# Performance work log

Hardware: AMD Instinct MI355X
Metric: run time of the kernel (lower is better)

## Reference

```python
import jax, jax.numpy as jnp
import numpy as np

B, L, E, D = 4, 4096, 768, 64

def setup_inputs() -> dict:
    key = jax.random.key(0)
    ks = jax.random.split(key, 7)
    x = jax.random.normal(ks[0], (B, L, E), dtype=jnp.float32)
    # True = masked (strict upper triangle), as in masked_fill semantics
    causal_mask = jnp.triu(jnp.ones((L, L), dtype=bool), k=1)
    # True = valid token (inverted with ~ inside forward); all valid to avoid NaN rows
    pad_mask = jnp.ones((B, L), dtype=bool)
    s = 1.0 / np.sqrt(E)
    Wk = jax.random.uniform(ks[1], (E, D), jnp.float32, -s, s)
    bk = jax.random.uniform(ks[2], (D,), jnp.float32, -s, s)
    Wq = jax.random.uniform(ks[3], (E, D), jnp.float32, -s, s)
    bq = jax.random.uniform(ks[4], (D,), jnp.float32, -s, s)
    Wv = jax.random.uniform(ks[5], (E, D), jnp.float32, -s, s)
    bv = jax.random.uniform(ks[6], (D,), jnp.float32, -s, s)
    return {"x": x, "causal_mask": causal_mask, "pad_mask": pad_mask,
            "Wk": Wk, "bk": bk, "Wq": Wq, "bq": bq, "Wv": Wv, "bv": bv}

def reference(x, causal_mask, pad_mask, Wk, bk, Wq, bq, Wv, bv):
    # Linear projections: [B,L,E] @ [E,D] + [D]
    K = jnp.einsum('ble,ed->bld', x, Wk) + bk
    Q = jnp.einsum('ble,ed->bld', x, Wq) + bq
    V = jnp.einsum('ble,ed->bld', x, Wv) + bv
    d = Q.shape[-1]
    scores = jnp.einsum('bqd,bkd->bqk', Q, K) / jnp.sqrt(jnp.asarray(d, Q.dtype))
    # full_mask: causal (True=masked) OR key-position padding (~pad_mask, broadcast over query dim)
    full_mask = causal_mask[None, :, :] | (~pad_mask)[:, None, :]
    scores = jnp.where(full_mask, -jnp.inf, scores)
    attn = jax.nn.softmax(scores, axis=-1)
    out = jnp.einsum('bqk,bkd->bqd', attn, V)
    return out
```

## Files before the change

### kernel.cpp

```cpp
#include <hip/hip_runtime.h>

#define L_SEQ 4096
#define BATCH 4
#define EDIM 768

typedef __attribute__((ext_vector_type(8))) short bf16x8;
typedef __attribute__((ext_vector_type(4))) float f32x4;
typedef __attribute__((ext_vector_type(16))) float f32x16;
typedef __attribute__((ext_vector_type(4))) unsigned short u16x4;
typedef __attribute__((ext_vector_type(8))) unsigned short u16x8;
typedef __attribute__((ext_vector_type(2))) _Float16 f16x2;
typedef __attribute__((ext_vector_type(4))) _Float16 f16x4;

#define QSCALE (0.125f * 1.4426950408889634f)

__device__ __forceinline__ unsigned short f2bf(float f) {
  unsigned u = __builtin_bit_cast(unsigned, f);
  u += 0x7FFFu + ((u >> 16) & 1u);
  return (unsigned short)(u >> 16);
}

__device__ __forceinline__ f16x4 half_of(u16x8 v, int h) {
  u16x4 t = h ? (u16x4){v[4], v[5], v[6], v[7]} : (u16x4){v[0], v[1], v[2], v[3]};
  return __builtin_bit_cast(f16x4, t);
}

__device__ __forceinline__ f16x2 pkrtz(float a, float b) {
  return __builtin_bit_cast(f16x2, __builtin_amdgcn_cvt_pkrtz(a, b));
}

__global__ __launch_bounds__(256) void prep_kernel(
    const float* __restrict__ Wq, const float* __restrict__ Wk,
    const float* __restrict__ Wv, unsigned short* __restrict__ WT) {
  int g = blockIdx.x * 256 + threadIdx.x;
  if (g >= 192 * EDIM) return;
  int row = g / EDIM, k = g - row * EDIM;
  int z = row >> 6, n = row & 63;
  const float* W = (z == 0) ? Wq : (z == 1) ? Wk : Wv;
  WT[g] = f2bf(W[k * 64 + n]);
}

__global__ __launch_bounds__(512) void proj_kernel(
    const float* __restrict__ x, const unsigned short* __restrict__ WT,
    const float* __restrict__ bq, const float* __restrict__ bk, const float* __restrict__ bv,
    unsigned short* __restrict__ Qf, unsigned short* __restrict__ Kf,
    unsigned short* __restrict__ Vf) {
  __shared__ unsigned short SH[2 * 13824];
  int tid = threadIdx.x;
  int w = tid >> 6, lane = tid & 63, l15 = lane & 15, g4 = lane >> 4;
  int rq = w & 3, ch = w >> 2;
  int m0 = blockIdx.x * 64;
  int brow = tid >> 3, bsg = tid & 7;

  f32x4 acc[6];
#pragma unroll
  for (int cf = 0; cf < 6; cf++) acc[cf] = (f32x4){0.f, 0.f, 0.f, 0.f};

  f32x4 arA[4], arB[4];
  u16x8 brA[3], brB[3];

  auto loadA = [&](f32x4 (&ar)[4], int k0) {
    const float* xp = x + (size_t)(m0 + 16 * rq + l15) * EDIM + k0 + g4 * 8;
    ar[0] = *(const f32x4*)xp;
    ar[1] = *(const f32x4*)(xp + 4);
    ar[2] = *(const f32x4*)(xp + 32);
    ar[3] = *(const f32x4*)(xp + 36);
  };
  auto loadB = [&](u16x8 (&br)[3], int k0) {
#pragma unroll
    for (int pp = 0; pp < 3; pp++)
      br[pp] = *(const u16x8*)(WT + (size_t)(brow + pp * 64) * EDIM + k0 + bsg * 8);
  };
  auto writeB = [&](int cur, u16x8 (&br)[3]) {
#pragma unroll
    for (int pp = 0; pp < 3; pp++)
      *(u16x8*)&SH[cur * 13824 + (brow + pp * 64) * 72 + bsg * 8] = br[pp];
  };
  auto mkfrag = [&](f32x4 lo, f32x4 hi) {
    union { u16x8 u; bf16x8 b; } r;
    r.u[0] = f2bf(lo[0]); r.u[1] = f2bf(lo[1]); r.u[2] = f2bf(lo[2]); r.u[3] = f2bf(lo[3]);
    r.u[4] = f2bf(hi[0]); r.u[5] = f2bf(hi[1]); r.u[6] = f2bf(hi[2]); r.u[7] = f2bf(hi[3]);
    return r.b;
  };
  auto compute = [&](int cur, f32x4 (&ar)[4]) {
#pragma unroll
    for (int ks = 0; ks < 2; ks++) {
      bf16x8 a = mkfrag(ar[ks * 2], ar[ks * 2 + 1]);
#pragma unroll
      for (int cf = 0; cf < 6; cf++) {
        bf16x8 bb = *(const bf16x8*)&SH[cur * 13824 + (ch * 96 + cf * 16 + l15) * 72 +
                                        ks * 32 + g4 * 8];
        acc[cf] = __builtin_amdgcn_mfma_f32_16x16x32_bf16(a, bb, acc[cf], 0, 0, 0);
      }
    }
  };

  loadA(arA, 0);
  loadB(brA, 0);
  for (int ss = 0; ss < 6; ss++) {
    int k1 = (2 * ss + 1) * 64;
    loadA(arB, k1);
    loadB(brB, k1);
    writeB(0, brA);
    __syncthreads();
    compute(0, arA);
    if (ss < 5) {
      int k2 = (2 * ss + 2) * 64;
      loadA(arA, k2);
      loadB(brA, k2);
    }
    writeB(1, brB);
    __syncthreads();
    compute(1, arB);
  }

  __syncthreads();
  unsigned short* LQ = SH;
  unsigned short* LK = SH + 4096;
  unsigned short* LV = SH + 8192;
#pragma unroll
  for (int cf = 0; cf < 6; cf++) {
    int c = ch * 96 + cf * 16 + l15;
    int z = c >> 6, d = c & 63;
    float bb_ = (z == 0) ? bq[d] : (z == 1) ? bk[d] : bv[d];
#pragma unroll
    for (int r = 0; r < 4; r++) {
      int t = 16 * rq + g4 * 4 + r;
      int sl = t >> 5, tl = t & 31;
      float v = acc[cf][r] + bb_;
      if (z == 2) {
        int fv = sl * 2048 + (d >> 5) * 1024 + ((tl >> 4) & 1) * 512 +
                 ((d & 31) + ((tl >> 2) & 1) * 32) * 8 + ((tl >> 3) & 1) * 4 + (tl & 3);
        _Float16 hv = (_Float16)v;
        LV[fv] = __builtin_bit_cast(unsigned short, hv);
      } else {
        int fqk = sl * 2048 + (d >> 4) * 512 + (tl + ((d >> 3) & 1) * 32) * 8 + (d & 7);
        if (z == 0) LQ[fqk] = f2bf(v * QSCALE);
        else        LK[fqk] = f2bf(v);
      }
    }
  }
  __syncthreads();
  {
    int b_ = m0 >> 12;
    int S0 = (m0 >> 5) & 127;
    size_t base = ((size_t)(b_ * 128 + S0)) * 2048;
    ((u16x8*)(Qf + base))[tid] = ((const u16x8*)LQ)[tid];
    ((u16x8*)(Kf + base))[tid] = ((const u16x8*)LK)[tid];
    ((u16x8*)(Vf + base))[tid] = ((const u16x8*)LV)[tid];
  }
}

__global__ __launch_bounds__(512, 2) void attn_kernel(
    const unsigned short* __restrict__ Qf, const unsigned short* __restrict__ Kf,
    const unsigned short* __restrict__ Vf, float* __restrict__ out) {
  __shared__ float OB[8][32][68];
  __shared__ float ML[8][2][32];
  int tid = threadIdx.x;
  int w = tid >> 6, lane = tid & 63;
  int ql = lane & 31, hi = lane >> 5;
  int blk = blockIdx.x;
  int xcd = blk & 7;
  int b = xcd >> 1;
  int pid = ((xcd & 1) << 5) | (blk >> 3);
  int sA = pid, sB = 127 - pid;
  size_t bL = (size_t)b * L_SEQ;
  const unsigned short* Qb = Qf + (size_t)b * 128 * 2048;
  const unsigned short* Kb = Kf + (size_t)b * 128 * 2048;
  const unsigned short* Vb = Vf + (size_t)b * 128 * 2048;

  bf16x8 qA[4], qB[4];
#pragma unroll
  for (int kh = 0; kh < 4; kh++) {
    qA[kh] = *(const bf16x8*)(Qb + ((size_t)sA * 4 + kh) * 512 + lane * 8);
    qB[kh] = *(const bf16x8*)(Qb + ((size_t)sB * 4 + kh) * 512 + lane * 8);
  }
  f32x16 oA0, oA1, oB0, oB1;
#pragma unroll
  for (int i = 0; i < 16; i++) { oA0[i] = 0.f; oA1[i] = 0.f; oB0[i] = 0.f; oB1[i] = 0.f; }
  float mA = -1e38f, lA = 0.f, mB = -1e38f, lB = 0.f;

  auto loadK = [&](bf16x8 (&kf)[4], int j) {
    const unsigned short* kp = Kb + (size_t)j * 2048 + lane * 8;
#pragma unroll
    for (int q = 0; q < 4; q++) kf[q] = *(const bf16x8*)(kp + q * 512);
  };
  auto loadV = [&](u16x8 (&vf)[4], int j) {
    const unsigned short* vp = Vb + (size_t)j * 2048 + lane * 8;
#pragma unroll
    for (int q = 0; q < 4; q++) vf[q] = *(const u16x8*)(vp + q * 512);
  };

  auto strip = [&](bf16x8 (&kf)[4], u16x8 (&vf)[4], int j, int s, bf16x8 (&qf)[4],
                   f32x16& o0, f32x16& o1, float& m, float& l) {
    f32x16 st;
#pragma unroll
    for (int i = 0; i < 16; i++) st[i] = 0.f;
    __builtin_amdgcn_s_setprio(1);
#pragma unroll
    for (int kh = 0; kh < 4; kh++)
      st = __builtin_amdgcn_mfma_f32_32x32x16_bf16(kf[kh], qf[kh], st, 0, 0, 0);
    __builtin_amdgcn_s_setprio(0);

    if (j == s) {
#pragma unroll
      for (int r = 0; r < 16; r++) {
        int tl = (r & 3) + 8 * (r >> 2) + 4 * hi;
        if (tl > ql) st[r] = -1e30f;
      }
    }

    float mx = st[0];
#pragma unroll
    for (int r = 1; r < 16; r++) mx = fmaxf(mx, st[r]);
    mx = fmaxf(mx, __shfl_xor(mx, 32));
    if (!__all(mx <= m + 11.0f)) {
      float mn = fmaxf(m, mx);
      float sc = exp2f(m - mn);
      m = mn; l *= sc;
#pragma unroll
      for (int i = 0; i < 16; i++) { o0[i] *= sc; o1[i] *= sc; }
    }
    float rs = 0.f;
#pragma unroll
    for (int r = 0; r < 16; r++) { st[r] = exp2f(st[r] - m); rs += st[r]; }
    rs += __shfl_xor(rs, 32);
    l += rs;

    f16x4 pb[4];
#pragma unroll
    for (int oc = 0; oc < 4; oc++) {
      f16x2 a = pkrtz(st[4 * oc], st[4 * oc + 1]);
      f16x2 c = pkrtz(st[4 * oc + 2], st[4 * oc + 3]);
      pb[oc] = (f16x4){a[0], a[1], c[0], c[1]};
    }
    __builtin_amdgcn_s_setprio(1);
#pragma unroll
    for (int oc = 0; oc < 4; oc++)
      o0 = __builtin_amdgcn_mfma_f32_32x32x8f16(half_of(vf[oc >> 1], oc & 1), pb[oc], o0, 0, 0, 0);
#pragma unroll
    for (int oc = 0; oc < 4; oc++)
      o1 = __builtin_amdgcn_mfma_f32_32x32x8f16(half_of(vf[2 + (oc >> 1)], oc & 1), pb[oc], o1, 0, 0, 0);
    __builtin_amdgcn_s_setprio(0);
  };

  bf16x8 kfA[4], kfB[4];
  u16x8 vfA[4], vfB[4];
  {
    int j = w;
    loadK(kfA, j);
    loadV(vfA, j);
    while (true) {
      int jn = j + 8;
      bool hasB = (jn <= sB);
      if (hasB) loadK(kfB, jn);
      if (j <= sA) strip(kfA, vfA, j, sA, qA, oA0, oA1, mA, lA);
      if (hasB) loadV(vfB, jn);
      strip(kfA, vfA, j, sB, qB, oB0, oB1, mB, lB);
      if (!hasB) break;
      j = jn;
      jn = j + 8;
      bool hasA = (jn <= sB);
      if (hasA) loadK(kfA, jn);
      if (j <= sA) strip(kfB, vfB, j, sA, qA, oA0, oA1, mA, lA);
      if (hasA) loadV(vfA, jn);
      strip(kfB, vfB, j, sB, qB, oB0, oB1, mB, lB);
      if (!hasA) break;
      j = jn;
    }
  }

  auto stash_reduce = [&](int s, f32x16& o0, f32x16& o1, float m, float l) {
    __syncthreads();
#pragma unroll
    for (int g = 0; g < 4; g++) {
      *(f32x4*)&OB[w][ql][8 * g + 4 * hi] =
          (f32x4){o0[4 * g], o0[4 * g + 1], o0[4 * g + 2], o0[4 * g + 3]};
      *(f32x4*)&OB[w][ql][32 + 8 * g + 4 * hi] =
          (f32x4){o1[4 * g], o1[4 * g + 1], o1[4 * g + 2], o1[4 * g + 3]};
    }
    if (hi == 0) { ML[w][0][ql] = m; ML[w][1][ql] = l; }
    __syncthreads();
    int q = tid >> 4, dg = tid & 15;
    float mw[8], lw[8];
    float ms = -1e38f;
#pragma unroll
    for (int ww = 0; ww < 8; ww++) {
      mw[ww] = ML[ww][0][q]; lw[ww] = ML[ww][1][q];
      ms = fmaxf(ms, mw[ww]);
    }
    float denom = 0.f, ew[8];
#pragma unroll
    for (int ww = 0; ww < 8; ww++) { ew[ww] = exp2f(mw[ww] - ms); denom += lw[ww] * ew[ww]; }
    float inv = 1.0f / denom;
    f32x4 acc = (f32x4){0.f, 0.f, 0.f, 0.f};
#pragma unroll
    for (int ww = 0; ww < 8; ww++) {
      f32x4 v = *(const f32x4*)&OB[ww][q][dg * 4];
      acc += v * ew[ww];
    }
    acc *= inv;
    *(f32x4*)(out + (bL + (size_t)s * 32 + q) * 64 + dg * 4) = acc;
  };
  stash_reduce(sA, oA0, oA1, mA, lA);
  stash_reduce(sB, oB0, oB1, mB, lB);
}

extern "C" void kernel_launch(void* const* d_in, const int* in_sizes, int n_in,
                              void* d_out, int out_size, void* d_ws, size_t ws_size,
                              hipStream_t stream) {
  const float* x  = (const float*)d_in[0];
  const float* Wk = (const float*)d_in[3];
  const float* bk = (const float*)d_in[4];
  const float* Wq = (const float*)d_in[5];
  const float* bq = (const float*)d_in[6];
  const float* Wv = (const float*)d_in[7];
  const float* bv = (const float*)d_in[8];
  float* out = (float*)d_out;

  char* ws = (char*)d_ws;
  unsigned short* WT = (unsigned short*)ws;
  unsigned short* Qf = (unsigned short*)(ws + 294912);
  unsigned short* Kf = (unsigned short*)(ws + 294912 + 2097152);
  unsigned short* Vf = (unsigned short*)(ws + 294912 + 2 * 2097152);

  prep_kernel<<<576, 256, 0, stream>>>(Wq, Wk, Wv, WT);
  proj_kernel<<<256, 512, 0, stream>>>(x, WT, bq, bk, bv, Qf, Kf, Vf);
  attn_kernel<<<256, 512, 0, stream>>>(Qf, Kf, Vf, out);
}
```

Measured before the change: 53.89 us.

## Load projection weights directly from global and switch softmax to natural exp

The projection kernel drops the LDS staging of bf16 weights and the per-stage barriers, reading B fragments straight from global/L2, and triple-buffers the x loads across a fully unrolled K loop. The Q scale no longer folds in log2(e); softmax uses __expf in place of exp2f and the rescale threshold drops from 11 to 8. The attention loop issues the K and V loads together rather than splitting them around the strips. This removes the LDS writes and syncs in the projection, but adds redundant global weight reads per wave and extra multiplies inside __expf, which lowers to exp2 of a scaled input.

```diff
diff --git a/kernel.cpp b/kernel.cpp
--- a/kernel.cpp
+++ b/kernel.cpp
@@ -11,8 +11,6 @@
 typedef __attribute__((ext_vector_type(8))) unsigned short u16x8;
 typedef __attribute__((ext_vector_type(2))) _Float16 f16x2;
 typedef __attribute__((ext_vector_type(4))) _Float16 f16x4;
-
-#define QSCALE (0.125f * 1.4426950408889634f)
 
 __device__ __forceinline__ unsigned short f2bf(float f) {
   unsigned u = __builtin_bit_cast(unsigned, f);
@@ -45,36 +43,26 @@
     const float* __restrict__ bq, const float* __restrict__ bk, const float* __restrict__ bv,
     unsigned short* __restrict__ Qf, unsigned short* __restrict__ Kf,
     unsigned short* __restrict__ Vf) {
-  __shared__ unsigned short SH[2 * 13824];
+  __shared__ unsigned short SH[12288];
   int tid = threadIdx.x;
   int w = tid >> 6, lane = tid & 63, l15 = lane & 15, g4 = lane >> 4;
   int rq = w & 3, ch = w >> 2;
   int m0 = blockIdx.x * 64;
-  int brow = tid >> 3, bsg = tid & 7;
 
   f32x4 acc[6];
 #pragma unroll
   for (int cf = 0; cf < 6; cf++) acc[cf] = (f32x4){0.f, 0.f, 0.f, 0.f};
 
-  f32x4 arA[4], arB[4];
-  u16x8 brA[3], brB[3];
+  f32x4 arA[4], arB[4], arC[4];
+  const float* xrow = x + (size_t)(m0 + 16 * rq + l15) * EDIM + g4 * 8;
+  const unsigned short* Wb = WT + (size_t)(ch * 96 + l15) * EDIM + g4 * 8;
 
   auto loadA = [&](f32x4 (&ar)[4], int k0) {
-    const float* xp = x + (size_t)(m0 + 16 * rq + l15) * EDIM + k0 + g4 * 8;
+    const float* xp = xrow + k0;
     ar[0] = *(const f32x4*)xp;
     ar[1] = *(const f32x4*)(xp + 4);
     ar[2] = *(const f32x4*)(xp + 32);
     ar[3] = *(const f32x4*)(xp + 36);
-  };
-  auto loadB = [&](u16x8 (&br)[3], int k0) {
-#pragma unroll
-    for (int pp = 0; pp < 3; pp++)
-      br[pp] = *(const u16x8*)(WT + (size_t)(brow + pp * 64) * EDIM + k0 + bsg * 8);
-  };
-  auto writeB = [&](int cur, u16x8 (&br)[3]) {
-#pragma unroll
-    for (int pp = 0; pp < 3; pp++)
-      *(u16x8*)&SH[cur * 13824 + (brow + pp * 64) * 72 + bsg * 8] = br[pp];
   };
   auto mkfrag = [&](f32x4 lo, f32x4 hi) {
     union { u16x8 u; bf16x8 b; } r;
@@ -82,39 +70,28 @@
     r.u[4] = f2bf(hi[0]); r.u[5] = f2bf(hi[1]); r.u[6] = f2bf(hi[2]); r.u[7] = f2bf(hi[3]);
     return r.b;
   };
-  auto compute = [&](int cur, f32x4 (&ar)[4]) {
+  auto compute = [&](f32x4 (&ar)[4], int k0) {
 #pragma unroll
     for (int ks = 0; ks < 2; ks++) {
       bf16x8 a = mkfrag(ar[ks * 2], ar[ks * 2 + 1]);
 #pragma unroll
       for (int cf = 0; cf < 6; cf++) {
-        bf16x8 bb = *(const bf16x8*)&SH[cur * 13824 + (ch * 96 + cf * 16 + l15) * 72 +
-                                        ks * 32 + g4 * 8];
+        bf16x8 bb = *(const bf16x8*)(Wb + (size_t)cf * 16 * EDIM + k0 + ks * 32);
         acc[cf] = __builtin_amdgcn_mfma_f32_16x16x32_bf16(a, bb, acc[cf], 0, 0, 0);
       }
     }
   };
 
   loadA(arA, 0);
-  loadB(brA, 0);
-  for (int ss = 0; ss < 6; ss++) {
-    int k1 = (2 * ss + 1) * 64;
-    loadA(arB, k1);
-    loadB(brB, k1);
-    writeB(0, brA);
-    __syncthreads();
-    compute(0, arA);
-    if (ss < 5) {
-      int k2 = (2 * ss + 2) * 64;
-      loadA(arA, k2);
-      loadB(brA, k2);
-    }
-    writeB(1, brB);
-    __syncthreads();
-    compute(1, arB);
-  }
-
-  __syncthreads();
+  loadA(arB, 64);
+#pragma unroll
+  for (int ss = 0; ss < 12; ss++) {
+    int r3 = ss % 3;
+    if (r3 == 0) { if (ss < 10) loadA(arC, (ss + 2) * 64); compute(arA, ss * 64); }
+    else if (r3 == 1) { if (ss < 10) loadA(arA, (ss + 2) * 64); compute(arB, ss * 64); }
+    else { if (ss < 10) loadA(arB, (ss + 2) * 64); compute(arC, ss * 64); }
+  }
+
   unsigned short* LQ = SH;
   unsigned short* LK = SH + 4096;
   unsigned short* LV = SH + 8192;
@@ -135,7 +112,7 @@
         LV[fv] = __builtin_bit_cast(unsigned short, hv);
       } else {
         int fqk = sl * 2048 + (d >> 4) * 512 + (tl + ((d >> 3) & 1) * 32) * 8 + (d & 7);
-        if (z == 0) LQ[fqk] = f2bf(v * QSCALE);
+        if (z == 0) LQ[fqk] = f2bf(v * 0.125f);
         else        LK[fqk] = f2bf(v);
       }
     }
@@ -180,13 +157,11 @@
   for (int i = 0; i < 16; i++) { oA0[i] = 0.f; oA1[i] = 0.f; oB0[i] = 0.f; oB1[i] = 0.f; }
   float mA = -1e38f, lA = 0.f, mB = -1e38f, lB = 0.f;
 
-  auto loadK = [&](bf16x8 (&kf)[4], int j) {
+  auto loadKV = [&](bf16x8 (&kf)[4], u16x8 (&vf)[4], int j) {
     const unsigned short* kp = Kb + (size_t)j * 2048 + lane * 8;
+    const unsigned short* vp = Vb + (size_t)j * 2048 + lane * 8;
 #pragma unroll
     for (int q = 0; q < 4; q++) kf[q] = *(const bf16x8*)(kp + q * 512);
-  };
-  auto loadV = [&](u16x8 (&vf)[4], int j) {
-    const unsigned short* vp = Vb + (size_t)j * 2048 + lane * 8;
 #pragma unroll
     for (int q = 0; q < 4; q++) vf[q] = *(const u16x8*)(vp + q * 512);
   };
@@ -214,16 +189,16 @@
 #pragma unroll
     for (int r = 1; r < 16; r++) mx = fmaxf(mx, st[r]);
     mx = fmaxf(mx, __shfl_xor(mx, 32));
-    if (!__all(mx <= m + 11.0f)) {
+    if (!__all(mx <= m + 8.0f)) {
       float mn = fmaxf(m, mx);
-      float sc = exp2f(m - mn);
+      float sc = __expf(m - mn);
       m = mn; l *= sc;
 #pragma unroll
       for (int i = 0; i < 16; i++) { o0[i] *= sc; o1[i] *= sc; }
     }
     float rs = 0.f;
 #pragma unroll
-    for (int r = 0; r < 16; r++) { st[r] = exp2f(st[r] - m); rs += st[r]; }
+    for (int r = 0; r < 16; r++) { st[r] = __expf(st[r] - m); rs += st[r]; }
     rs += __shfl_xor(rs, 32);
     l += rs;
 
@@ -244,27 +219,27 @@
     __builtin_amdgcn_s_setprio(0);
   };
 
+  auto step = [&](bf16x8 (&kf)[4], u16x8 (&vf)[4], int j) {
+    if (j <= sA) strip(kf, vf, j, sA, qA, oA0, oA1, mA, lA);
+    strip(kf, vf, j, sB, qB, oB0, oB1, mB, lB);
+  };
+
   bf16x8 kfA[4], kfB[4];
   u16x8 vfA[4], vfB[4];
   {
     int j = w;
-    loadK(kfA, j);
-    loadV(vfA, j);
+    loadKV(kfA, vfA, j);
     while (true) {
       int jn = j + 8;
       bool hasB = (jn <= sB);
-      if (hasB) loadK(kfB, jn);
-      if (j <= sA) strip(kfA, vfA, j, sA, qA, oA0, oA1, mA, lA);
-      if (hasB) loadV(vfB, jn);
-      strip(kfA, vfA, j, sB, qB, oB0, oB1, mB, lB);
+      if (hasB) loadKV(kfB, vfB, jn);
+      step(kfA, vfA, j);
       if (!hasB) break;
       j = jn;
       jn = j + 8;
       bool hasA = (jn <= sB);
-      if (hasA) loadK(kfA, jn);
-      if (j <= sA) strip(kfB, vfB, j, sA, qA, oA0, oA1, mA, lA);
-      if (hasA) loadV(vfA, jn);
-      strip(kfB, vfB, j, sB, qB, oB0, oB1, mB, lB);
+      if (hasA) loadKV(kfA, vfA, jn);
+      step(kfB, vfB, j);
       if (!hasA) break;
       j = jn;
     }
@@ -291,7 +266,7 @@
     }
     float denom = 0.f, ew[8];
 #pragma unroll
-    for (int ww = 0; ww < 8; ww++) { ew[ww] = exp2f(mw[ww] - ms); denom += lw[ww] * ew[ww]; }
+    for (int ww = 0; ww < 8; ww++) { ew[ww] = __expf(mw[ww] - ms); denom += lw[ww] * ew[ww]; }
     float inv = 1.0f / denom;
     f32x4 acc = (f32x4){0.f, 0.f, 0.f, 0.f};
 #pragma unroll
```

Measured after the change: 75.49 us. 40.1% more time.
